# Kernel optimization log

Hardware: AMD Instinct MI355X
Metric: run time of the kernel (lower is better)

Reference implementation:

```python
import jax, jax.numpy as jnp
import numpy as np

EPS = 1e-12  # matches torch.nn.functional.normalize eps


def _l2_normalize(x):
    n = jnp.linalg.norm(x, axis=-1, keepdims=True)
    return x / jnp.maximum(n, EPS)


def setup_inputs() -> dict:
    key = jax.random.key(0)
    k1, k2, k3, k4 = jax.random.split(key, 4)
    N, D = 8192, 1024
    return {
        "query_ids": jax.random.randint(k1, (N,), 0, 1000, dtype=jnp.int64 if jax.config.jax_enable_x64 else jnp.int32),
        "key_ids": jax.random.randint(k2, (N,), 0, 1000, dtype=jnp.int64 if jax.config.jax_enable_x64 else jnp.int32),
        "query_embed": jax.random.normal(k3, (N, D), dtype=jnp.float32),
        "key_embed": jax.random.normal(k4, (N, D), dtype=jnp.float32),
        "k": 5,
    }


def reference(query_ids, key_ids, query_embed, key_embed, k):
    q = _l2_normalize(query_embed)          # [N, D]
    kb = _l2_normalize(key_embed)           # [N, D]
    sims = q @ kb.T                          # [N, N] cosine similarities
    # argsort(descending)[1:k+1] == top-(k+1) indices, dropping the best match
    _, idx = jax.lax.top_k(sims, k + 1)      # [N, k+1]
    idx = idx[:, 1:]                         # [N, k]
    matched = (key_ids[idx] == query_ids[:, None]).astype(jnp.float32)  # [N, k]
    # mean over k per row, then mean over rows == global mean (equal row sizes)
    return jnp.mean(matched)
```

## Files before the change

### kernel.cpp

```cpp
#include <hip/hip_runtime.h>
#include <math.h>

#define NROWS 8192
#define DIM   1024
#define KDIM  1024
#define KSEL  5
#define TOPK  6
#define QB    256
#define KBB   256
#define NKB   (NROWS / KBB)
#define NQB   (NROWS / QB)
#define PS    51

typedef __attribute__((ext_vector_type(8))) short bf16x8;
typedef __attribute__((ext_vector_type(4))) float f32x4;


__device__ __forceinline__ unsigned short f2bf(float x) {
    unsigned u = __float_as_uint(x);
    unsigned r = (u + 0x7fffu + ((u >> 16) & 1u)) >> 16;
    return (unsigned short)r;
}

__device__ __forceinline__ bool better(float v, int id, float v2, int id2) {
    return (v > v2) || (v == v2 && id < id2);
}
__device__ __forceinline__ void insert6(float v, int id, float* tv, int* ti) {
    if (!better(v, id, tv[TOPK - 1], ti[TOPK - 1])) return;
    int j = TOPK - 1;
    while (j > 0 && better(v, id, tv[j - 1], ti[j - 1])) {
        tv[j] = tv[j - 1]; ti[j] = ti[j - 1]; --j;
    }
    tv[j] = v; ti[j] = id;
}

__device__ __forceinline__ void ins6(float v, int id, float* tv, int* ti) {
    if (v <= tv[5]) return;
    bool gt[6];
#pragma unroll
    for (int j = 0; j < 6; ++j) gt[j] = v > tv[j];
#pragma unroll
    for (int j = 5; j >= 1; --j)
        if (gt[j - 1]) { tv[j] = tv[j - 1]; ti[j] = ti[j - 1]; }
    if (gt[0]) { tv[0] = v; ti[0] = id; }
#pragma unroll
    for (int j = 1; j < 6; ++j)
        if (gt[j] && !gt[j - 1]) { tv[j] = v; ti[j] = id; }
}

__device__ __forceinline__ void async16(const unsigned short* g, unsigned short* l) {
    __builtin_amdgcn_global_load_lds(
        (const __attribute__((address_space(1))) void*)g,
        (__attribute__((address_space(3))) void*)l, 16, 0, 0);
}

__global__ __launch_bounds__(128) void prep_kernel(
        const float* __restrict__ q, const float* __restrict__ kb,
        unsigned short* __restrict__ Q2, unsigned short* __restrict__ K2) {
    const int b = blockIdx.x;
    const bool isQ = (b < NROWS);
    const int r = isQ ? b : b - NROWS;
    const float* src = (isQ ? q : kb) + (size_t)r * DIM;
    unsigned short* D = (isQ ? Q2 : K2) + (size_t)r * KDIM;

    const int t = threadIdx.x;
    float4 v0 = *(const float4*)(src + t * 4);
    float4 v1 = *(const float4*)(src + 512 + t * 4);
    float s = v0.x * v0.x + v0.y * v0.y + v0.z * v0.z + v0.w * v0.w
            + v1.x * v1.x + v1.y * v1.y + v1.z * v1.z + v1.w * v1.w;
    for (int o = 32; o; o >>= 1) s += __shfl_down(s, o, 64);
    __shared__ float wsum[2];
    __shared__ float inv_s;
    int lane = t & 63, wid = t >> 6;
    if (lane == 0) wsum[wid] = s;
    __syncthreads();
    if (t == 0)
        inv_s = 1.0f / fmaxf(sqrtf(wsum[0] + wsum[1]), 1e-12f);
    __syncthreads();
    const float inv = inv_s;

    float xs[8] = {v0.x * inv, v0.y * inv, v0.z * inv, v0.w * inv,
                   v1.x * inv, v1.y * inv, v1.z * inv, v1.w * inv};
    bf16x8 hi;
#pragma unroll
    for (int i = 0; i < 8; ++i)
        hi[i] = (short)f2bf(xs[i]);
    const int off = (t >> 3) * 64 + (((t & 7) ^ (r & 7)) * 8);
    *(bf16x8*)(D + off) = hi;
}

__global__ __launch_bounds__(512, 2) void gemm_topk_kernel(
        const unsigned short* __restrict__ Q2, const unsigned short* __restrict__ K2,
        float2* __restrict__ partials) {
    __shared__ __align__(16) char smem[131072];
    float2* mbuf = (float2*)smem;

    const int tid = threadIdx.x;
    const int w = tid >> 6, l = tid & 63;
    const int l15 = l & 15, l4 = l >> 4;
    const int qbase = blockIdx.x * QB;
    const int kbase = blockIdx.y * KBB;
    const int wkh = w & 1;
    const int wqh = w >> 1;

    const int arow  = tid >> 3;
    const int akoff = (tid & 7) * 8;

    const int xr = l15 & 7;
    const int fa_row = (wkh * 128 + l15) * 64;
    const int fb_row = (wqh * 64 + l15) * 64;

    const size_t qstage = (size_t)(qbase + arow) * KDIM + akoff;
    const size_t kstage = (size_t)(kbase + arow) * KDIM + akoff;

    f32x4 acc[8][4];
#pragma unroll
    for (int mt = 0; mt < 8; ++mt)
#pragma unroll
        for (int nt = 0; nt < 4; ++nt) acc[mt][nt] = (f32x4){0.f, 0.f, 0.f, 0.f};

    {
        unsigned short* Ksb = (unsigned short*)smem;
        unsigned short* Qsb = Ksb + 16384;
#pragma unroll
        for (int j = 0; j < 4; ++j)
            async16(K2 + kstage + (size_t)j * 64 * KDIM,
                    Ksb + (tid + j * 512) * 8);
#pragma unroll
        for (int j = 0; j < 4; ++j)
            async16(Q2 + qstage + (size_t)j * 64 * KDIM,
                    Qsb + (tid + j * 512) * 8);
    }
    __syncthreads();

    int cur = 0;
#pragma unroll 1
    for (int k0 = 0; k0 < KDIM; k0 += 64) {
        unsigned short* Ksb = (unsigned short*)(smem + (cur << 16));
        unsigned short* Qsb = Ksb + 16384;

        const int nk0 = k0 + 64;
        if (nk0 < KDIM) {
            unsigned short* Ksn = (unsigned short*)(smem + ((cur ^ 1) << 16));
            unsigned short* Qsn = Ksn + 16384;
#pragma unroll
            for (int j = 0; j < 4; ++j)
                async16(K2 + kstage + (size_t)j * 64 * KDIM + nk0,
                        Ksn + (tid + j * 512) * 8);
#pragma unroll
            for (int j = 0; j < 4; ++j)
                async16(Q2 + qstage + (size_t)j * 64 * KDIM + nk0,
                        Qsn + (tid + j * 512) * 8);
        }

#pragma unroll
        for (int ks = 0; ks < 2; ++ks) {
            const int p8 = ((ks * 4 + l4) ^ xr) * 8;
            bf16x8 af[8], bfr[4];
#pragma unroll
            for (int mt = 0; mt < 8; ++mt)
                af[mt] = *(const bf16x8*)(Ksb + fa_row + mt * 1024 + p8);
#pragma unroll
            for (int nt = 0; nt < 4; ++nt)
                bfr[nt] = *(const bf16x8*)(Qsb + fb_row + nt * 1024 + p8);
            __builtin_amdgcn_s_setprio(1);
#pragma unroll
            for (int mt = 0; mt < 8; ++mt)
#pragma unroll
                for (int nt = 0; nt < 4; ++nt)
                    acc[mt][nt] = __builtin_amdgcn_mfma_f32_16x16x32_bf16(
                        af[mt], bfr[nt], acc[mt][nt], 0, 0, 0);
            __builtin_amdgcn_s_setprio(0);
        }

        __syncthreads();
        cur ^= 1;
    }

    float tvl[4][6]; int til[4][6];
#pragma unroll
    for (int n = 0; n < 4; ++n)
#pragma unroll
        for (int i = 0; i < 6; ++i) { tvl[n][i] = -INFINITY; til[n][i] = 0x7fffffff; }

#pragma unroll
    for (int nt = 0; nt < 4; ++nt) {
#pragma unroll
        for (int mt = 0; mt < 8; ++mt) {
            const f32x4 a = acc[mt][nt];
            const float m4 = fmaxf(fmaxf(a.x, a.y), fmaxf(a.z, a.w));
            if (m4 > tvl[nt][5]) {
                const int kk = kbase + wkh * 128 + mt * 16 + l4 * 4;
                ins6(a.x, kk + 0, tvl[nt], til[nt]);
                ins6(a.y, kk + 1, tvl[nt], til[nt]);
                ins6(a.z, kk + 2, tvl[nt], til[nt]);
                ins6(a.w, kk + 3, tvl[nt], til[nt]);
            }
        }
    }

    __syncthreads();
    const int slot = wkh * 4 + l4;
#pragma unroll
    for (int nt = 0; nt < 4; ++nt) {
        const int ql = wqh * 64 + nt * 16 + l15;
        float2* dst = mbuf + (size_t)ql * PS + slot * 6;
#pragma unroll
        for (int e = 0; e < 6; ++e)
            dst[e] = make_float2(tvl[nt][e], __int_as_float(til[nt][e]));
    }
    __syncthreads();

    if (tid < 256) {
        float tv[6]; int ti[6];
#pragma unroll
        for (int i = 0; i < 6; ++i) { tv[i] = -INFINITY; ti[i] = 0x7fffffff; }
        const float2* src = mbuf + (size_t)tid * PS;
        for (int e = 0; e < 48; ++e) {
            float2 p = src[e];
            if (p.x < tv[5]) continue;
            insert6(p.x, __float_as_int(p.y), tv, ti);
        }
        size_t off = ((size_t)(qbase + tid) * NKB + blockIdx.y) * TOPK;
#pragma unroll
        for (int i = 0; i < 6; ++i)
            partials[off + i] = make_float2(tv[i], __int_as_float(ti[i]));
    }
}

__global__ __launch_bounds__(256) void merge_kernel(
        const float2* __restrict__ partials,
        const int* __restrict__ query_ids, const int* __restrict__ key_ids,
        int* __restrict__ counter, int* __restrict__ done,
        float* __restrict__ out) {
    __shared__ float2 lbuf[32][49];
    __shared__ int sc[32];
    const int tid  = threadIdx.x;
    const int rloc = tid >> 3;
    const int part = tid & 7;
    const int row  = blockIdx.x * 32 + rloc;

    float tv[6]; int ti[6];
#pragma unroll
    for (int i = 0; i < 6; ++i) { tv[i] = -INFINITY; ti[i] = 0x7fffffff; }
    const float2* src = partials + ((size_t)row * NKB + part * 4) * TOPK;
#pragma unroll
    for (int e = 0; e < 24; ++e) {
        float2 p = src[e];
        if (p.x < tv[5]) continue;
        insert6(p.x, __float_as_int(p.y), tv, ti);
    }
#pragma unroll
    for (int i = 0; i < 6; ++i)
        lbuf[rloc][part * 6 + i] = make_float2(tv[i], __int_as_float(ti[i]));
    __syncthreads();

    if (part == 0) {
        float tv2[6]; int ti2[6];
#pragma unroll
        for (int i = 0; i < 6; ++i) { tv2[i] = -INFINITY; ti2[i] = 0x7fffffff; }
#pragma unroll
        for (int e = 0; e < 48; ++e) {
            float2 p = lbuf[rloc][e];
            if (p.x < tv2[5]) continue;
            insert6(p.x, __float_as_int(p.y), tv2, ti2);
        }
        const int qid = query_ids[row];
        int cnt = 0;
#pragma unroll
        for (int r = 1; r < TOPK; ++r)
            cnt += (key_ids[ti2[r]] == qid) ? 1 : 0;
        sc[rloc] = cnt;
    }
    __syncthreads();
    if (tid == 0) {
        int c = 0;
#pragma unroll
        for (int i = 0; i < 32; ++i) c += sc[i];
        atomicAdd(counter, c);
        __threadfence();
        int prev = atomicAdd(done, 1);
        if (prev == gridDim.x - 1) {
            int total = atomicAdd(counter, 0);
            out[0] = (float)total / (float)(NROWS * KSEL);
        }
    }
}

extern "C" void kernel_launch(void* const* d_in, const int* in_sizes, int n_in,
                              void* d_out, int out_size, void* d_ws, size_t ws_size,
                              hipStream_t stream) {
    (void)in_sizes; (void)n_in; (void)out_size; (void)ws_size;
    const int*   query_ids = (const int*)d_in[0];
    const int*   key_ids   = (const int*)d_in[1];
    const float* q         = (const float*)d_in[2];
    const float* kb        = (const float*)d_in[3];

    char* ws = (char*)d_ws;
    const size_t MB16 = (size_t)NROWS * KDIM * sizeof(unsigned short);
    int*            counter  = (int*)ws;
    unsigned short* Q2       = (unsigned short*)(ws + 256);
    unsigned short* K2       = (unsigned short*)(ws + 256 + MB16);
    float2*         partials = (float2*)(ws + 256 + 2 * MB16);

    hipMemsetAsync(counter, 0, 2 * sizeof(int), stream);
    prep_kernel<<<2 * NROWS, 128, 0, stream>>>(q, kb, Q2, K2);
    gemm_topk_kernel<<<dim3(NQB, NKB), 512, 0, stream>>>(Q2, K2, partials);
    merge_kernel<<<NROWS / 32, 256, 0, stream>>>(partials, query_ids, key_ids,
                                                 counter, counter + 1,
                                                 (float*)d_out);
}
```

Before: 353.2 us.

## Prefetch two K-tiles ahead with partial vmcnt waits in GEMM main loop

Restructures the double-buffered main loop so the first two 64-wide K tiles are preloaded. Each iteration then issues loads for tile t+2 into the buffer just consumed and waits only until the older group of async loads has landed (vmcnt(8)), not draining all of them with __syncthreads. This is meant to keep more global loads in flight and hide latency behind the MFMA work. In exchange it adds an extra barrier per iteration and relies on hand-written waitcnt counts that must match the number of async16 loads issued.

New measurement: 362.8 us. 2.7% more time.

```diff
diff --git a/kernel.cpp b/kernel.cpp
--- a/kernel.cpp
+++ b/kernel.cpp
@@ -10,6 +10,7 @@
 #define KBB   256
 #define NKB   (NROWS / KBB)
 #define NQB   (NROWS / QB)
+#define NT    (KDIM / 64)
 #define PS    51
 
 typedef __attribute__((ext_vector_type(8))) short bf16x8;
@@ -120,38 +121,32 @@
         for (int nt = 0; nt < 4; ++nt) acc[mt][nt] = (f32x4){0.f, 0.f, 0.f, 0.f};
 
     {
-        unsigned short* Ksb = (unsigned short*)smem;
-        unsigned short* Qsb = Ksb + 16384;
+        unsigned short* K0 = (unsigned short*)smem;
+        unsigned short* Q0 = K0 + 16384;
+        unsigned short* K1 = (unsigned short*)(smem + 65536);
+        unsigned short* Q1 = K1 + 16384;
 #pragma unroll
         for (int j = 0; j < 4; ++j)
-            async16(K2 + kstage + (size_t)j * 64 * KDIM,
-                    Ksb + (tid + j * 512) * 8);
+            async16(K2 + kstage + (size_t)j * 64 * KDIM, K0 + (tid + j * 512) * 8);
 #pragma unroll
         for (int j = 0; j < 4; ++j)
-            async16(Q2 + qstage + (size_t)j * 64 * KDIM,
-                    Qsb + (tid + j * 512) * 8);
-    }
-    __syncthreads();
-
-    int cur = 0;
+            async16(Q2 + qstage + (size_t)j * 64 * KDIM, Q0 + (tid + j * 512) * 8);
+#pragma unroll
+        for (int j = 0; j < 4; ++j)
+            async16(K2 + kstage + (size_t)j * 64 * KDIM + 64, K1 + (tid + j * 512) * 8);
+#pragma unroll
+        for (int j = 0; j < 4; ++j)
+            async16(Q2 + qstage + (size_t)j * 64 * KDIM + 64, Q1 + (tid + j * 512) * 8);
+    }
+    asm volatile("s_waitcnt vmcnt(8)" ::: "memory");
+    __builtin_amdgcn_s_barrier();
+    __builtin_amdgcn_sched_barrier(0);
+
 #pragma unroll 1
-    for (int k0 = 0; k0 < KDIM; k0 += 64) {
+    for (int t = 0; t < NT; ++t) {
+        const int cur = t & 1;
         unsigned short* Ksb = (unsigned short*)(smem + (cur << 16));
         unsigned short* Qsb = Ksb + 16384;
-
-        const int nk0 = k0 + 64;
-        if (nk0 < KDIM) {
-            unsigned short* Ksn = (unsigned short*)(smem + ((cur ^ 1) << 16));
-            unsigned short* Qsn = Ksn + 16384;
-#pragma unroll
-            for (int j = 0; j < 4; ++j)
-                async16(K2 + kstage + (size_t)j * 64 * KDIM + nk0,
-                        Ksn + (tid + j * 512) * 8);
-#pragma unroll
-            for (int j = 0; j < 4; ++j)
-                async16(Q2 + qstage + (size_t)j * 64 * KDIM + nk0,
-                        Qsn + (tid + j * 512) * 8);
-        }
 
 #pragma unroll
         for (int ks = 0; ks < 2; ++ks) {
@@ -173,8 +168,28 @@
             __builtin_amdgcn_s_setprio(0);
         }
 
-        __syncthreads();
-        cur ^= 1;
+        __builtin_amdgcn_sched_barrier(0);
+        __builtin_amdgcn_s_barrier();
+        __builtin_amdgcn_sched_barrier(0);
+
+        if (t + 2 < NT) {
+            const int nk0 = (t + 2) * 64;
+#pragma unroll
+            for (int j = 0; j < 4; ++j)
+                async16(K2 + kstage + (size_t)j * 64 * KDIM + nk0,
+                        Ksb + (tid + j * 512) * 8);
+#pragma unroll
+            for (int j = 0; j < 4; ++j)
+                async16(Q2 + qstage + (size_t)j * 64 * KDIM + nk0,
+                        Qsb + (tid + j * 512) * 8);
+            asm volatile("s_waitcnt vmcnt(8)" ::: "memory");
+            __builtin_amdgcn_s_barrier();
+            __builtin_amdgcn_sched_barrier(0);
+        } else if (t + 1 < NT) {
+            asm volatile("s_waitcnt vmcnt(0)" ::: "memory");
+            __builtin_amdgcn_s_barrier();
+            __builtin_amdgcn_sched_barrier(0);
+        }
     }
 
     float tvl[4][6]; int til[4][6];
```
